# Performance work log

Hardware: AMD Instinct MI355X
Metric: run time of the kernel (lower is better)

## Reference

```python
import jax, jax.numpy as jnp
import numpy as np

N_NODES = 50000
N_EDGES = 800000
NEG_SLOPE = 0.2  # GATConv default
BN_EPS = 1e-5


def _seg_softmax(logits, seg, n):
    # per-target-node softmax over incoming edges (PyG softmax w/ +1e-16)
    m = jax.ops.segment_max(logits, seg, num_segments=n)
    m = jnp.where(jnp.isfinite(m), m, 0.0)
    e = jnp.exp(logits - m[seg])
    s = jax.ops.segment_sum(e, seg, num_segments=n)
    return e / (s[seg] + 1e-16)


def _gat_conv(x, src, dst, W, a_src, a_dst, b, concat):
    # x: [N, Fin]; W: [Fin, H*C]; a_src/a_dst: [H, C]
    n = x.shape[0]
    H, C = a_src.shape
    h = (x @ W).reshape(n, H, C)
    al_s = jnp.einsum('nhc,hc->nh', h, a_src)
    al_d = jnp.einsum('nhc,hc->nh', h, a_dst)
    logits = jax.nn.leaky_relu(al_s[src] + al_d[dst], NEG_SLOPE)  # [E, H]
    alpha = _seg_softmax(logits, dst, n)                           # [E, H]
    out = jax.ops.segment_sum(h[src] * alpha[:, :, None], dst, num_segments=n)
    out = out.reshape(n, H * C) if concat else out.mean(axis=1)
    return out + b


def _bn(x, g, b):
    mu = jnp.mean(x, axis=0)
    var = jnp.mean((x - mu) ** 2, axis=0)
    return (x - mu) * jax.lax.rsqrt(var + BN_EPS) * g + b


def _gat_params(key, fin, heads, ch, scale=0.1):
    k1, k2, k3 = jax.random.split(key, 3)
    W = jax.random.normal(k1, (fin, heads * ch), jnp.float32) * scale
    a_s = jax.random.normal(k2, (heads, ch), jnp.float32) * scale
    a_d = jax.random.normal(k3, (heads, ch), jnp.float32) * scale
    return W, a_s, a_d


def setup_inputs() -> dict:
    key = jax.random.key(0)
    ks = jax.random.split(key, 12)
    inp = {}
    inp['x'] = jax.random.normal(ks[0], (N_NODES, 3), jnp.float32)
    inp['edge_index'] = jax.random.randint(ks[1], (2, N_EDGES), 0, N_NODES, jnp.int64 if jax.config.jax_enable_x64 else jnp.int32)
    inp['W11'], inp['as11'], inp['ad11'] = _gat_params(ks[2], 3, 8, 8)
    inp['b11'] = jnp.zeros((64,), jnp.float32)
    inp['W12'], inp['as12'], inp['ad12'] = _gat_params(ks[3], 64, 8, 8)
    inp['b12'] = jnp.zeros((64,), jnp.float32)
    inp['g1'] = jnp.ones((64,), jnp.float32)
    inp['be1'] = jnp.zeros((64,), jnp.float32)
    inp['W21'], inp['as21'], inp['ad21'] = _gat_params(ks[4], 64, 8, 32)
    inp['b21'] = jnp.zeros((256,), jnp.float32)
    inp['W22'], inp['as22'], inp['ad22'] = _gat_params(ks[5], 256, 8, 32)
    inp['b22'] = jnp.zeros((256,), jnp.float32)
    inp['g2'] = jnp.ones((256,), jnp.float32)
    inp['be2'] = jnp.zeros((256,), jnp.float32)
    inp['W31'], inp['as31'], inp['ad31'] = _gat_params(ks[6], 256, 8, 64)
    inp['b31'] = jnp.zeros((512,), jnp.float32)
    inp['W32'], inp['as32'], inp['ad32'] = _gat_params(ks[7], 512, 8, 1)
    inp['b32'] = jnp.zeros((1,), jnp.float32)
    return inp


def reference(x, edge_index,
              W11, as11, ad11, b11, W12, as12, ad12, b12, g1, be1,
              W21, as21, ad21, b21, W22, as22, ad22, b22, g2, be2,
              W31, as31, ad31, b31, W32, as32, ad32, b32):
    n = x.shape[0]
    loops = jnp.arange(n, dtype=edge_index.dtype)
    src = jnp.concatenate([edge_index[0], loops])  # add_self_loops=True
    dst = jnp.concatenate([edge_index[1], loops])
    # GAT(3, 64, 2): conv -> relu -> conv
    h = jax.nn.relu(_gat_conv(x, src, dst, W11, as11, ad11, b11, True))
    h = _gat_conv(h, src, dst, W12, as12, ad12, b12, True)
    h = jax.nn.leaky_relu(_bn(h, g1, be1), 0.1)
    # GAT(64, 256, 2)
    h = jax.nn.relu(_gat_conv(h, src, dst, W21, as21, ad21, b21, True))
    h = _gat_conv(h, src, dst, W22, as22, ad22, b22, True)
    h = jax.nn.leaky_relu(_bn(h, g2, be2), 0.1)
    # GAT(256, 512, 2, 1): conv -> relu -> conv(concat=False)
    h = jax.nn.relu(_gat_conv(h, src, dst, W31, as31, ad31, b31, True))
    h = _gat_conv(h, src, dst, W32, as32, ad32, b32, False)
    return jax.nn.sigmoid(h)
```

## Files before the change

kernel.cpp:

```cpp
#include <hip/hip_runtime.h>
#include <math.h>

typedef short short8 __attribute__((ext_vector_type(8)));
typedef short short4v __attribute__((ext_vector_type(4)));
typedef float f32x4 __attribute__((ext_vector_type(4)));

__device__ __forceinline__ unsigned short f2bf(float v){
  unsigned u = __builtin_bit_cast(unsigned, v);
  u += 0x7FFFu + ((u >> 16) & 1u);
  return (unsigned short)(u >> 16);
}
__device__ __forceinline__ float bf2f(unsigned short b){
  unsigned u = ((unsigned)b) << 16;
  return __builtin_bit_cast(float, u);
}

__global__ void k_deg(const int* __restrict__ dstv, int* __restrict__ deg, int E){
  int e = blockIdx.x*blockDim.x + threadIdx.x;
  if (e < E) atomicAdd(&deg[dstv[e]], 1);
}

__global__ void k_scan(const int* __restrict__ deg, int* __restrict__ off,
                       int* __restrict__ cursor, int N){
  __shared__ int wpre[16];
  __shared__ int s_tot;
  __shared__ int carry;
  int tid = threadIdx.x;
  int lane = tid & 63, wv = tid >> 6;
  if (tid == 0) carry = 0;
  __syncthreads();
  for (int base = 0; base < N; base += 1024){
    int i = base + tid;
    int v = (i < N) ? deg[i] : 0;
    int incl = v;
    #pragma unroll
    for (int d = 1; d < 64; d <<= 1){
      int t = __shfl_up(incl, d, 64);
      if (lane >= d) incl += t;
    }
    if (lane == 63) wpre[wv] = incl;
    __syncthreads();
    if (tid < 16){
      int x = wpre[tid];
      int ix = x;
      #pragma unroll
      for (int d = 1; d < 16; d <<= 1){
        int t = __shfl_up(ix, d, 16);
        if (tid >= d) ix += t;
      }
      wpre[tid] = ix - x;
      if (tid == 15) s_tot = ix;
    }
    __syncthreads();
    int c = carry;
    int excl = c + wpre[wv] + (incl - v);
    if (i < N){ off[i+1] = excl + v; cursor[i] = excl; }
    __syncthreads();
    if (tid == 0) carry = c + s_tot;
    __syncthreads();
  }
  if (tid == 0) off[0] = 0;
}

__global__ void k_fill(const int* __restrict__ srcv, const int* __restrict__ dstv,
                       int* __restrict__ cursor, int* __restrict__ csr, int E){
  int e = blockIdx.x*blockDim.x + threadIdx.x;
  if (e < E){
    int d = dstv[e];
    int p = atomicAdd(&cursor[d], 1);
    csr[p] = srcv[e];
  }
}

__global__ void k_prepB(const float* __restrict__ W, unsigned short* __restrict__ bh,
                        unsigned short* __restrict__ bl, int K, int kpshift, int Nn){
  int Kp = 1 << kpshift;
  int i = blockIdx.x*blockDim.x + threadIdx.x;
  if (i >= Nn*Kp) return;
  int n = i >> kpshift, k = i & (Kp-1);
  float v = (k < K) ? W[(size_t)k*Nn + n] : 0.0f;
  unsigned short h = f2bf(v);
  bh[i] = h;
  bl[i] = f2bf(v - bf2f(h));
}

__global__ void k_bn_coef(const float* __restrict__ bsum, const float* __restrict__ bsq,
                          const float* __restrict__ g, const float* __restrict__ b,
                          float* __restrict__ sc, float* __restrict__ sh,
                          float invN, int HC){
  int f = threadIdx.x + blockIdx.x*blockDim.x;
  if (f >= HC) return;
  float mu  = bsum[f]*invN;
  float var = bsq[f]*invN - mu*mu;
  float rs  = rsqrtf(var + 1e-5f) * g[f];
  sc[f] = rs;
  sh[f] = b[f] - mu*rs;
}

template<int BN, int MODE>
__global__ __launch_bounds__((BN==64)?256:512)
void gemm_mfma(const float* __restrict__ A, const unsigned short* __restrict__ Bh,
               const unsigned short* __restrict__ Bl,
               const float* __restrict__ bnsc, const float* __restrict__ bnsh,
               const float* __restrict__ a_s, const float* __restrict__ a_d,
               unsigned short* __restrict__ Pb, float* __restrict__ D, int M, int K){
  constexpr int WAVES   = (BN==64) ? 4 : 8;
  constexpr int BLOCK   = WAVES*64;
  constexpr int WAVES_N = BN/64;
  constexpr int WAVES_M = WAVES/WAVES_N;
  constexpr int WM      = 64/WAVES_M;
  constexpr int MF      = WM/16;
  constexpr int CH      = (BN==512)?64 : (BN==256)?32 : 8;
  const int Kp = (K + 63) & ~(int)63;

  __shared__ char lds[16384];

  int tid  = threadIdx.x;
  int lane = tid & 63;
  int wid  = tid >> 6;
  int wn = wid % WAVES_N;
  int wm = wid / WAVES_N;
  int n0w = wn*64;
  int wm0 = wm*WM;
  int m0 = blockIdx.x * 64;

  f32x4 acc[MF][4];
  #pragma unroll
  for (int i = 0; i < MF; ++i)
    #pragma unroll
    for (int j = 0; j < 4; ++j)
      acc[i][j] = (f32x4){0.f,0.f,0.f,0.f};

  constexpr int SITER = 512/BLOCK;

  for (int k0 = 0; k0 < Kp; k0 += 64){
    __syncthreads();
    #pragma unroll
    for (int it = 0; it < SITER; ++it){
      int i = it*BLOCK + tid;
      int row = i >> 3, c8 = i & 7;
      int gm = m0 + row;
      int gk = k0 + c8*8;
      float v[8];
      if (gm < M && gk + 8 <= K){
        const float* ap = A + (size_t)gm*K + gk;
        float4 x0 = *(const float4*)ap;
        float4 x1 = *(const float4*)(ap+4);
        v[0]=x0.x; v[1]=x0.y; v[2]=x0.z; v[3]=x0.w;
        v[4]=x1.x; v[5]=x1.y; v[6]=x1.z; v[7]=x1.w;
        if constexpr (MODE == 1){
          #pragma unroll
          for (int j=0;j<8;++j){
            float u = v[j]*bnsc[gk+j] + bnsh[gk+j];
            v[j] = u > 0.f ? u : 0.1f*u;
          }
        }
      } else {
        #pragma unroll
        for (int j=0;j<8;++j){
          int gkj = gk + j;
          bool ok = (gm < M && gkj < K);
          float u = ok ? A[(size_t)gm*K + gkj] : 0.0f;
          if constexpr (MODE == 1){
            if (ok){
              u = u*bnsc[gkj] + bnsh[gkj];
              u = u > 0.f ? u : 0.1f*u;
            }
          }
          v[j] = u;
        }
      }
      short8 hi, lo;
      #pragma unroll
      for (int j=0;j<8;++j){
        unsigned short hb = f2bf(v[j]);
        hi[j] = (short)hb;
        lo[j] = (short)f2bf(v[j] - bf2f(hb));
      }
      int off = row*128 + ((c8 ^ (row&7))<<4);
      *(short8*)(lds + off) = hi;
      *(short8*)(lds + 8192 + off) = lo;
    }
    __syncthreads();
    #pragma unroll
    for (int kk = 0; kk < 2; ++kk){
      short8 bhf[4], blf[4];
      #pragma unroll
      for (int nf = 0; nf < 4; ++nf){
        int ncol = n0w + nf*16 + (lane & 15);
        int kidx = k0 + kk*32 + ((lane>>4)<<3);
        size_t bo = (size_t)ncol*Kp + kidx;
        bhf[nf] = *(const short8*)(Bh + bo);
        blf[nf] = *(const short8*)(Bl + bo);
      }
      #pragma unroll
      for (int mt = 0; mt < MF; ++mt){
        int row = wm0 + mt*16 + (lane & 15);
        int c8 = kk*4 + (lane>>4);
        int off = row*128 + ((c8 ^ (row&7))<<4);
        short8 ah = *(const short8*)(lds + off);
        short8 al = *(const short8*)(lds + 8192 + off);
        #pragma unroll
        for (int nf = 0; nf < 4; ++nf){
          acc[mt][nf] = __builtin_amdgcn_mfma_f32_16x16x32_bf16(ah, bhf[nf], acc[mt][nf], 0,0,0);
          acc[mt][nf] = __builtin_amdgcn_mfma_f32_16x16x32_bf16(ah, blf[nf], acc[mt][nf], 0,0,0);
          acc[mt][nf] = __builtin_amdgcn_mfma_f32_16x16x32_bf16(al, bhf[nf], acc[mt][nf], 0,0,0);
        }
      }
    }
  }

  float asv[4], adv[4];
  #pragma unroll
  for (int nf=0; nf<4; ++nf){
    int gcol = n0w + nf*16 + (lane&15);
    asv[nf] = a_s[gcol];
    adv[nf] = a_d[gcol];
  }
  #pragma unroll
  for (int mt = 0; mt < MF; ++mt){
    #pragma unroll
    for (int r = 0; r < 4; ++r){
      int gm = m0 + wm0 + mt*16 + ((lane>>4)<<2) + r;
      bool ok = gm < M;
      #pragma unroll
      for (int nf=0;nf<4;++nf){
        if (ok) Pb[(size_t)gm*BN + n0w + nf*16 + (lane&15)] = f2bf(acc[mt][nf][r]);
      }
      float* dp = D + (size_t)gm*16;
      if constexpr (CH == 64){
        float ps = acc[mt][0][r]*asv[0] + acc[mt][1][r]*asv[1]
                 + acc[mt][2][r]*asv[2] + acc[mt][3][r]*asv[3];
        float pd = acc[mt][0][r]*adv[0] + acc[mt][1][r]*adv[1]
                 + acc[mt][2][r]*adv[2] + acc[mt][3][r]*adv[3];
        #pragma unroll
        for (int d2=1; d2<16; d2<<=1){ ps += __shfl_xor(ps,d2,64); pd += __shfl_xor(pd,d2,64); }
        if (ok && (lane&15)==0){
          int head = n0w >> 6;
          dp[head] = ps;
          dp[8 + head] = pd;
        }
      } else if constexpr (CH == 32){
        float ps0 = acc[mt][0][r]*asv[0] + acc[mt][1][r]*asv[1];
        float ps1 = acc[mt][2][r]*asv[2] + acc[mt][3][r]*asv[3];
        float pd0 = acc[mt][0][r]*adv[0] + acc[mt][1][r]*adv[1];
        float pd1 = acc[mt][2][r]*adv[2] + acc[mt][3][r]*adv[3];
        #pragma unroll
        for (int d2=1; d2<16; d2<<=1){
          ps0 += __shfl_xor(ps0,d2,64); ps1 += __shfl_xor(ps1,d2,64);
          pd0 += __shfl_xor(pd0,d2,64); pd1 += __shfl_xor(pd1,d2,64);
        }
        if (ok && (lane&15)==0){
          int head = n0w >> 5;
          dp[head]     = ps0;
          dp[head + 1] = ps1;
          dp[8 + head]     = pd0;
          dp[8 + head + 1] = pd1;
        }
      } else {
        #pragma unroll
        for (int nf=0;nf<4;++nf){
          float ps = acc[mt][nf][r]*asv[nf];
          float pd = acc[mt][nf][r]*adv[nf];
          #pragma unroll
          for (int d2=1; d2<8; d2<<=1){ ps += __shfl_xor(ps,d2,64); pd += __shfl_xor(pd,d2,64); }
          if (ok && (lane&7)==0){
            int head = nf*2 + ((lane>>3)&1);
            dp[head]     = ps;
            dp[8 + head] = pd;
          }
        }
      }
    }
  }
}

template<int HC, int ACT, int OBF>
__global__ __launch_bounds__(256)
void k_agg(const unsigned short* __restrict__ Pb, const float* __restrict__ D,
           const int* __restrict__ off, const int* __restrict__ csr,
           const float* __restrict__ bias, void* __restrict__ outv, int N){
  constexpr int R = HC/64;
  __shared__ float salpha[4][512];
  int lane = threadIdx.x & 63;
  int wid  = threadIdx.x >> 6;
  int n = blockIdx.x*4 + wid;
  if (n >= N) return;
  int o0 = off[n], deg = off[n+1]-o0;
  int myh = lane >> 3;

  float aldn[8];
  {
    const float* dn = D + (size_t)n*16 + 8;
    float4 x0 = *(const float4*)dn;
    float4 x1 = *(const float4*)(dn+4);
    aldn[0]=x0.x; aldn[1]=x0.y; aldn[2]=x0.z; aldn[3]=x0.w;
    aldn[4]=x1.x; aldn[5]=x1.y; aldn[6]=x1.z; aldn[7]=x1.w;
  }

  float acc[R];
  #pragma unroll
  for (int j=0;j<R;++j) acc[j]=0.f;

  if (deg < 64){
    int nE = deg + 1;
    int myidx = (lane < deg) ? csr[o0+lane] : n;
    bool active = (lane < nE);
    float v[8];
    {
      const float* dp = D + (size_t)myidx*16;
      float4 x0 = *(const float4*)dp;
      float4 x1 = *(const float4*)(dp+4);
      float t[8] = {x0.x,x0.y,x0.z,x0.w,x1.x,x1.y,x1.z,x1.w};
      #pragma unroll
      for (int h=0;h<8;++h){
        float u = t[h] + aldn[h];
        u = u > 0.f ? u : 0.2f*u;
        v[h] = active ? u : -1e30f;
      }
    }
    float m[8];
    #pragma unroll
    for (int h=0;h<8;++h) m[h]=v[h];
    #pragma unroll
    for (int d=1; d<64; d<<=1)
      #pragma unroll
      for (int h=0;h<8;++h) m[h] = fmaxf(m[h], __shfl_xor(m[h], d, 64));
    float sv[8], s[8];
    #pragma unroll
    for (int h=0;h<8;++h){ sv[h] = active ? __expf(v[h]-m[h]) : 0.f; s[h]=sv[h]; }
    #pragma unroll
    for (int d=1; d<64; d<<=1)
      #pragma unroll
      for (int h=0;h<8;++h) s[h] += __shfl_xor(s[h], d, 64);
    if (active){
      #pragma unroll
      for (int h=0;h<8;++h) salpha[wid][lane*8+h] = sv[h] / (s[h] + 1e-16f);
    }
    asm volatile("s_waitcnt lgkmcnt(0)" ::: "memory");

    for (int e=0; e<nE; ++e){
      int src = __shfl(myidx, e, 64);
      float alpha = salpha[wid][e*8 + myh];
      const unsigned short* hp = Pb + (size_t)src*HC + lane*R;
      if constexpr (R == 1){
        acc[0] += alpha * bf2f(hp[0]);
      } else if constexpr (R == 4){
        short4v w = *(const short4v*)hp;
        #pragma unroll
        for (int j=0;j<4;++j) acc[j] += alpha * bf2f((unsigned short)w[j]);
      } else {
        short8 w = *(const short8*)hp;
        #pragma unroll
        for (int j=0;j<8;++j) acc[j] += alpha * bf2f((unsigned short)w[j]);
      }
    }
  } else {
    float m[8];
    #pragma unroll
    for (int h=0;h<8;++h) m[h] = -1e30f;
    for (int e = lane; e <= deg; e += 64){
      int src = (e < deg) ? csr[o0+e] : n;
      const float* ap = D + (size_t)src*16;
      #pragma unroll
      for (int h=0;h<8;++h){
        float u = ap[h] + aldn[h];
        u = u > 0.f ? u : 0.2f*u;
        m[h] = fmaxf(m[h], u);
      }
    }
    #pragma unroll
    for (int d=1; d<64; d<<=1)
      #pragma unroll
      for (int h=0;h<8;++h) m[h] = fmaxf(m[h], __shfl_xor(m[h], d, 64));
    float s[8] = {0,0,0,0,0,0,0,0};
    for (int e = lane; e <= deg; e += 64){
      int src = (e < deg) ? csr[o0+e] : n;
      const float* ap = D + (size_t)src*16;
      #pragma unroll
      for (int h=0;h<8;++h){
        float u = ap[h] + aldn[h];
        u = u > 0.f ? u : 0.2f*u;
        s[h] += __expf(u - m[h]);
      }
    }
    #pragma unroll
    for (int d=1; d<64; d<<=1)
      #pragma unroll
      for (int h=0;h<8;++h) s[h] += __shfl_xor(s[h], d, 64);
    float mh = m[myh];
    float rsh = 1.0f/(s[myh] + 1e-16f);
    float adh = aldn[myh];
    for (int e = 0; e <= deg; ++e){
      int src = (e < deg) ? csr[o0+e] : n;
      float u = D[(size_t)src*16 + myh] + adh;
      u = u > 0.f ? u : 0.2f*u;
      float alpha = __expf(u - mh) * rsh;
      const unsigned short* hp = Pb + (size_t)src*HC + lane*R;
      if constexpr (R == 1){
        acc[0] += alpha * bf2f(hp[0]);
      } else if constexpr (R == 4){
        short4v w = *(const short4v*)hp;
        #pragma unroll
        for (int j=0;j<4;++j) acc[j] += alpha * bf2f((unsigned short)w[j]);
      } else {
        short8 w = *(const short8*)hp;
        #pragma unroll
        for (int j=0;j<8;++j) acc[j] += alpha * bf2f((unsigned short)w[j]);
      }
    }
  }

  #pragma unroll
  for (int j = 0; j < R; ++j){
    int f = lane*R + j;
    float v = acc[j] + bias[f];
    if (ACT == 1) v = fmaxf(v, 0.0f);
    if constexpr (OBF == 1)
      ((unsigned short*)outv)[(size_t)n*HC + f] = f2bf(v);
    else
      ((float*)outv)[(size_t)n*HC + f] = v;
  }
}

__global__ void k_bn_stats(const float* __restrict__ x, float* __restrict__ gsum,
                           float* __restrict__ gsq, int N, int HC){
  int f = threadIdx.x;
  float s = 0.f, q = 0.f;
  for (int r = blockIdx.x; r < N; r += gridDim.x){
    float v = x[(size_t)r*HC + f];
    s += v; q += v*v;
  }
  atomicAdd(&gsum[f], s);
  atomicAdd(&gsq[f], q);
}

__global__ __launch_bounds__(256)
void gemm8(const unsigned short* __restrict__ Qb, const float* __restrict__ W,
           float* __restrict__ h8, int M){
  int lane = threadIdx.x & 63;
  int gw = (blockIdx.x*blockDim.x + threadIdx.x) >> 6;
  int nw = (gridDim.x*blockDim.x) >> 6;
  float w[8][8];
  const float* wp = W + lane*64;
  #pragma unroll
  for (int j=0;j<8;++j){
    float4 a = *(const float4*)(wp + j*8);
    float4 b = *(const float4*)(wp + j*8 + 4);
    w[j][0]=a.x; w[j][1]=a.y; w[j][2]=a.z; w[j][3]=a.w;
    w[j][4]=b.x; w[j][5]=b.y; w[j][6]=b.z; w[j][7]=b.w;
  }
  for (int n = gw; n < M; n += nw){
    short8 v8 = *(const short8*)(Qb + (size_t)n*512 + lane*8);
    float p[8] = {0,0,0,0,0,0,0,0};
    #pragma unroll
    for (int j=0;j<8;++j){
      float x = bf2f((unsigned short)v8[j]);
      #pragma unroll
      for (int o=0;o<8;++o) p[o] += x * w[j][o];
    }
    #pragma unroll
    for (int d=1; d<64; d<<=1)
      #pragma unroll
      for (int o=0;o<8;++o) p[o] += __shfl_xor(p[o], d, 64);
    if (lane == 0){
      float4 y0 = make_float4(p[0],p[1],p[2],p[3]);
      float4 y1 = make_float4(p[4],p[5],p[6],p[7]);
      *(float4*)(h8 + (size_t)n*8)     = y0;
      *(float4*)(h8 + (size_t)n*8 + 4) = y1;
    }
  }
}

__global__ __launch_bounds__(256)
void k_final(const float* __restrict__ h8, const float* __restrict__ a_s,
             const float* __restrict__ a_d, const int* __restrict__ off,
             const int* __restrict__ csr, const float* __restrict__ b32,
             float* __restrict__ outp, int N){
  int lane = threadIdx.x & 63;
  int wv   = threadIdx.x >> 6;
  int n = blockIdx.x*4 + wv;
  if (n >= N) return;
  int o0 = off[n], deg = off[n+1]-o0;
  float asv[8], adv[8];
  #pragma unroll
  for (int h=0;h<8;++h){ asv[h]=a_s[h]; adv[h]=a_d[h]; }
  float aldn[8];
  {
    const float* hp = h8 + (size_t)n*8;
    float4 x0 = *(const float4*)hp;
    float4 x1 = *(const float4*)(hp+4);
    float hn[8] = {x0.x,x0.y,x0.z,x0.w,x1.x,x1.y,x1.z,x1.w};
    #pragma unroll
    for (int h=0;h<8;++h) aldn[h] = hn[h]*adv[h];
  }

  if (deg < 64){
    int nE = deg + 1;
    int src = (lane < deg) ? csr[o0+lane] : n;
    bool act = (lane < nE);
    float hs[8];
    {
      const float* hp = h8 + (size_t)src*8;
      float4 x0 = *(const float4*)hp;
      float4 x1 = *(const float4*)(hp+4);
      hs[0]=x0.x; hs[1]=x0.y; hs[2]=x0.z; hs[3]=x0.w;
      hs[4]=x1.x; hs[5]=x1.y; hs[6]=x1.z; hs[7]=x1.w;
    }
    float v[8];
    #pragma unroll
    for (int h=0;h<8;++h){
      float u = hs[h]*asv[h] + aldn[h];
      u = u > 0.f ? u : 0.2f*u;
      v[h] = act ? u : -1e30f;
    }
    float m[8];
    #pragma unroll
    for (int h=0;h<8;++h) m[h]=v[h];
    #pragma unroll
    for (int d=1; d<64; d<<=1)
      #pragma unroll
      for (int h=0;h<8;++h) m[h] = fmaxf(m[h], __shfl_xor(m[h], d, 64));
    float s[8], t[8];
    #pragma unroll
    for (int h=0;h<8;++h){
      float e = act ? __expf(v[h]-m[h]) : 0.f;
      s[h]=e; t[h]=e*hs[h];
    }
    #pragma unroll
    for (int d=1; d<64; d<<=1)
      #pragma unroll
      for (int h=0;h<8;++h){
        s[h] += __shfl_xor(s[h], d, 64);
        t[h] += __shfl_xor(t[h], d, 64);
      }
    if (lane == 0){
      float o = 0.f;
      #pragma unroll
      for (int h=0;h<8;++h) o += t[h]/(s[h]+1e-16f);
      o = o*0.125f + b32[0];
      outp[n] = 1.0f/(1.0f + __expf(-o));
    }
  } else if (lane == 0){
    float m[8], s[8], agg[8];
    #pragma unroll
    for (int h=0;h<8;++h){ m[h]=-1e30f; s[h]=0.f; agg[h]=0.f; }
    for (int e = 0; e <= deg; ++e){
      int src = (e < deg) ? csr[o0+e] : n;
      #pragma unroll
      for (int h=0;h<8;++h){
        float u = h8[(size_t)src*8+h]*asv[h] + aldn[h];
        u = u > 0.f ? u : 0.2f*u;
        m[h] = fmaxf(m[h], u);
      }
    }
    for (int e = 0; e <= deg; ++e){
      int src = (e < deg) ? csr[o0+e] : n;
      #pragma unroll
      for (int h=0;h<8;++h){
        float u = h8[(size_t)src*8+h]*asv[h] + aldn[h];
        u = u > 0.f ? u : 0.2f*u;
        float ex = __expf(u - m[h]);
        s[h] += ex;
        agg[h] += ex * h8[(size_t)src*8+h];
      }
    }
    float o = 0.f;
    #pragma unroll
    for (int h=0;h<8;++h) o += agg[h]/(s[h]+1e-16f);
    o = o*0.125f + b32[0];
    outp[n] = 1.0f/(1.0f + __expf(-o));
  }
}

extern "C" void kernel_launch(void* const* d_in, const int* in_sizes, int n_in,
                              void* d_out, int out_size, void* d_ws, size_t ws_size,
                              hipStream_t stream){
  int N = in_sizes[0]/3;
  int E = in_sizes[1]/2;
  const float* x    = (const float*)d_in[0];
  const int*   ei   = (const int*)  d_in[1];
  const float* W11  = (const float*)d_in[2];
  const float* as11 = (const float*)d_in[3];
  const float* ad11 = (const float*)d_in[4];
  const float* b11  = (const float*)d_in[5];
  const float* W12  = (const float*)d_in[6];
  const float* as12 = (const float*)d_in[7];
  const float* ad12 = (const float*)d_in[8];
  const float* b12  = (const float*)d_in[9];
  const float* g1   = (const float*)d_in[10];
  const float* be1  = (const float*)d_in[11];
  const float* W21  = (const float*)d_in[12];
  const float* as21 = (const float*)d_in[13];
  const float* ad21 = (const float*)d_in[14];
  const float* b21  = (const float*)d_in[15];
  const float* W22  = (const float*)d_in[16];
  const float* as22 = (const float*)d_in[17];
  const float* ad22 = (const float*)d_in[18];
  const float* b22  = (const float*)d_in[19];
  const float* g2   = (const float*)d_in[20];
  const float* be2  = (const float*)d_in[21];
  const float* W31  = (const float*)d_in[22];
  const float* as31 = (const float*)d_in[23];
  const float* ad31 = (const float*)d_in[24];
  const float* b31  = (const float*)d_in[25];
  const float* W32  = (const float*)d_in[26];
  const float* as32 = (const float*)d_in[27];
  const float* ad32 = (const float*)d_in[28];
  const float* b32  = (const float*)d_in[29];

  char* ws = (char*)d_ws;
  size_t o = 0;
  auto alloc = [&](size_t bytes)->char*{
    char* p = ws + o;
    o = (o + bytes + 255) & ~(size_t)255;
    return p;
  };
  int*   deg    = (int*)  alloc((size_t)N*4);
  int*   off    = (int*)  alloc((size_t)(N+1)*4);
  int*   cursor = (int*)  alloc((size_t)N*4);
  int*   csr    = (int*)  alloc((size_t)E*4);
  unsigned short* bth = (unsigned short*)alloc(131072*2);
  unsigned short* btl = (unsigned short*)alloc(131072*2);
  float* h8     = (float*)alloc((size_t)N*8*4);
  float* bsum   = (float*)alloc(1024);
  float* bsq    = (float*)alloc(1024);
  float* bnsc   = (float*)alloc(1024);
  float* bnsh   = (float*)alloc(1024);
  unsigned short* Pb = (unsigned short*)alloc((size_t)N*512*2);
  float* D      = (float*)alloc((size_t)N*16*4);
  float* Q      = (float*)alloc((size_t)N*512*4);
  unsigned short* Qb = (unsigned short*)alloc((size_t)N*512*2);
  (void)ws_size;

  hipMemsetAsync(deg, 0, (size_t)N*4, stream);
  int eb = (E+255)/256;
  k_deg <<<eb, 256, 0, stream>>>(ei+E, deg, E);
  k_scan<<<1, 1024, 0, stream>>>(deg, off, cursor, N);
  k_fill<<<eb, 256, 0, stream>>>(ei, ei+E, cursor, csr, E);

  int mb = (N+63)/64;
  int nb4 = (N+3)/4;
  float invN = 1.0f/(float)N;

  k_prepB<<<(64*64)/256, 256, 0, stream>>>(W11, bth, btl, 3, 6, 64);
  gemm_mfma<64,0><<<mb, 256, 0, stream>>>(x, bth, btl, nullptr, nullptr,
                                          as11, ad11, Pb, D, N, 3);
  k_agg<64,1,0><<<nb4, 256, 0, stream>>>(Pb, D, off, csr, b11, Q, N);

  k_prepB<<<(64*64)/256, 256, 0, stream>>>(W12, bth, btl, 64, 6, 64);
  gemm_mfma<64,0><<<mb, 256, 0, stream>>>(Q, bth, btl, nullptr, nullptr,
                                          as12, ad12, Pb, D, N, 64);
  k_agg<64,0,0><<<nb4, 256, 0, stream>>>(Pb, D, off, csr, b12, Q, N);
  hipMemsetAsync(bsum, 0, 2048, stream);
  k_bn_stats<<<512, 64, 0, stream>>>(Q, bsum, bsq, N, 64);
  k_bn_coef<<<1, 64, 0, stream>>>(bsum, bsq, g1, be1, bnsc, bnsh, invN, 64);

  k_prepB<<<(256*64)/256, 256, 0, stream>>>(W21, bth, btl, 64, 6, 256);
  gemm_mfma<256,1><<<mb, 512, 0, stream>>>(Q, bth, btl, bnsc, bnsh,
                                           as21, ad21, Pb, D, N, 64);
  k_agg<256,1,0><<<nb4, 256, 0, stream>>>(Pb, D, off, csr, b21, Q, N);

  k_prepB<<<(256*256)/256, 256, 0, stream>>>(W22, bth, btl, 256, 8, 256);
  gemm_mfma<256,0><<<mb, 512, 0, stream>>>(Q, bth, btl, nullptr, nullptr,
                                           as22, ad22, Pb, D, N, 256);
  k_agg<256,0,0><<<nb4, 256, 0, stream>>>(Pb, D, off, csr, b22, Q, N);
  hipMemsetAsync(bsum, 0, 2048, stream);
  k_bn_stats<<<512, 256, 0, stream>>>(Q, bsum, bsq, N, 256);
  k_bn_coef<<<1, 256, 0, stream>>>(bsum, bsq, g2, be2, bnsc, bnsh, invN, 256);

  k_prepB<<<(512*256)/256, 256, 0, stream>>>(W31, bth, btl, 256, 8, 512);
  gemm_mfma<512,1><<<mb, 512, 0, stream>>>(Q, bth, btl, bnsc, bnsh,
                                           as31, ad31, Pb, D, N, 256);
  k_agg<512,1,1><<<nb4, 256, 0, stream>>>(Pb, D, off, csr, b31, Qb, N);

  gemm8<<<1024, 256, 0, stream>>>(Qb, W32, h8, N);
  k_final<<<nb4, 256, 0, stream>>>(h8, as32, ad32, off, csr, b32,
                                   (float*)d_out, N);
}
```

Baseline: 1.146 ms.

## Store intermediate activations in bf16 and split attention-logit buffers

All aggregation outputs are now written as bf16 instead of fp32. The following GEMMs read bf16 activations directly. When the input is already bf16 and needs no batchnorm transform, the GEMM drops the low-part A term, going from three MFMA passes to two and halving LDS use. The source and destination logit arrays are split into two contiguous 8-float buffers, so the edge gathers touch only source-logit rows. This cuts activation memory traffic and MFMA work, but activations and batchnorm statistics now carry bf16 rounding, which lowers accuracy.

```diff
diff --git a/kernel.cpp b/kernel.cpp
--- a/kernel.cpp
+++ b/kernel.cpp
@@ -97,13 +97,14 @@
   sh[f] = b[f] - mu*rs;
 }
 
-template<int BN, int MODE>
+template<int BN, int AFMT>
 __global__ __launch_bounds__((BN==64)?256:512)
-void gemm_mfma(const float* __restrict__ A, const unsigned short* __restrict__ Bh,
+void gemm_mfma(const void* __restrict__ Av, const unsigned short* __restrict__ Bh,
                const unsigned short* __restrict__ Bl,
                const float* __restrict__ bnsc, const float* __restrict__ bnsh,
                const float* __restrict__ a_s, const float* __restrict__ a_d,
-               unsigned short* __restrict__ Pb, float* __restrict__ D, int M, int K){
+               unsigned short* __restrict__ Pb, float* __restrict__ Ds,
+               float* __restrict__ Dd, int M, int K){
   constexpr int WAVES   = (BN==64) ? 4 : 8;
   constexpr int BLOCK   = WAVES*64;
   constexpr int WAVES_N = BN/64;
@@ -111,9 +112,10 @@
   constexpr int WM      = 64/WAVES_M;
   constexpr int MF      = WM/16;
   constexpr int CH      = (BN==512)?64 : (BN==256)?32 : 8;
+  constexpr int TERMS   = (AFMT==2) ? 2 : 3;
   const int Kp = (K + 63) & ~(int)63;
 
-  __shared__ char lds[16384];
+  __shared__ char lds[(TERMS==3)?16384:8192];
 
   int tid  = threadIdx.x;
   int lane = tid & 63;
@@ -141,45 +143,52 @@
       int row = i >> 3, c8 = i & 7;
       int gm = m0 + row;
       int gk = k0 + c8*8;
-      float v[8];
-      if (gm < M && gk + 8 <= K){
-        const float* ap = A + (size_t)gm*K + gk;
-        float4 x0 = *(const float4*)ap;
-        float4 x1 = *(const float4*)(ap+4);
-        v[0]=x0.x; v[1]=x0.y; v[2]=x0.z; v[3]=x0.w;
-        v[4]=x1.x; v[5]=x1.y; v[6]=x1.z; v[7]=x1.w;
-        if constexpr (MODE == 1){
+      int off = row*128 + ((c8 ^ (row&7))<<4);
+      if constexpr (AFMT == 2){
+        short8 hv = {0,0,0,0,0,0,0,0};
+        if (gm < M) hv = *(const short8*)((const unsigned short*)Av + (size_t)gm*K + gk);
+        *(short8*)(lds + off) = hv;
+      } else if constexpr (AFMT == 1){
+        short8 raw = {0,0,0,0,0,0,0,0};
+        if (gm < M) raw = *(const short8*)((const unsigned short*)Av + (size_t)gm*K + gk);
+        short8 hi, lo;
+        #pragma unroll
+        for (int j=0;j<8;++j){
+          float u = bf2f((unsigned short)raw[j])*bnsc[gk+j] + bnsh[gk+j];
+          u = u > 0.f ? u : 0.1f*u;
+          if (gm >= M) u = 0.f;
+          unsigned short hb = f2bf(u);
+          hi[j] = (short)hb;
+          lo[j] = (short)f2bf(u - bf2f(hb));
+        }
+        *(short8*)(lds + off) = hi;
+        *(short8*)(lds + 8192 + off) = lo;
+      } else {
+        const float* A = (const float*)Av;
+        float v[8];
+        if (gm < M && gk + 8 <= K){
+          const float* ap = A + (size_t)gm*K + gk;
+          float4 x0 = *(const float4*)ap;
+          float4 x1 = *(const float4*)(ap+4);
+          v[0]=x0.x; v[1]=x0.y; v[2]=x0.z; v[3]=x0.w;
+          v[4]=x1.x; v[5]=x1.y; v[6]=x1.z; v[7]=x1.w;
+        } else {
           #pragma unroll
           for (int j=0;j<8;++j){
-            float u = v[j]*bnsc[gk+j] + bnsh[gk+j];
-            v[j] = u > 0.f ? u : 0.1f*u;
+            int gkj = gk + j;
+            v[j] = (gm < M && gkj < K) ? A[(size_t)gm*K + gkj] : 0.0f;
           }
         }
-      } else {
+        short8 hi, lo;
         #pragma unroll
         for (int j=0;j<8;++j){
-          int gkj = gk + j;
-          bool ok = (gm < M && gkj < K);
-          float u = ok ? A[(size_t)gm*K + gkj] : 0.0f;
-          if constexpr (MODE == 1){
-            if (ok){
-              u = u*bnsc[gkj] + bnsh[gkj];
-              u = u > 0.f ? u : 0.1f*u;
-            }
-          }
-          v[j] = u;
-        }
-      }
-      short8 hi, lo;
-      #pragma unroll
-      for (int j=0;j<8;++j){
-        unsigned short hb = f2bf(v[j]);
-        hi[j] = (short)hb;
-        lo[j] = (short)f2bf(v[j] - bf2f(hb));
-      }
-      int off = row*128 + ((c8 ^ (row&7))<<4);
-      *(short8*)(lds + off) = hi;
-      *(short8*)(lds + 8192 + off) = lo;
+          unsigned short hb = f2bf(v[j]);
+          hi[j] = (short)hb;
+          lo[j] = (short)f2bf(v[j] - bf2f(hb));
+        }
+        *(short8*)(lds + off) = hi;
+        *(short8*)(lds + 8192 + off) = lo;
+      }
     }
     __syncthreads();
     #pragma unroll
@@ -199,12 +208,16 @@
         int c8 = kk*4 + (lane>>4);
         int off = row*128 + ((c8 ^ (row&7))<<4);
         short8 ah = *(const short8*)(lds + off);
-        short8 al = *(const short8*)(lds + 8192 + off);
         #pragma unroll
         for (int nf = 0; nf < 4; ++nf){
           acc[mt][nf] = __builtin_amdgcn_mfma_f32_16x16x32_bf16(ah, bhf[nf], acc[mt][nf], 0,0,0);
           acc[mt][nf] = __builtin_amdgcn_mfma_f32_16x16x32_bf16(ah, blf[nf], acc[mt][nf], 0,0,0);
-          acc[mt][nf] = __builtin_amdgcn_mfma_f32_16x16x32_bf16(al, bhf[nf], acc[mt][nf], 0,0,0);
+        }
+        if constexpr (TERMS == 3){
+          short8 al = *(const short8*)(lds + 8192 + off);
+          #pragma unroll
+          for (int nf = 0; nf < 4; ++nf)
+            acc[mt][nf] = __builtin_amdgcn_mfma_f32_16x16x32_bf16(al, bhf[nf], acc[mt][nf], 0,0,0);
         }
       }
     }
@@ -227,7 +240,6 @@
       for (int nf=0;nf<4;++nf){
         if (ok) Pb[(size_t)gm*BN + n0w + nf*16 + (lane&15)] = f2bf(acc[mt][nf][r]);
       }
-      float* dp = D + (size_t)gm*16;
       if constexpr (CH == 64){
         float ps = acc[mt][0][r]*asv[0] + acc[mt][1][r]*asv[1]
                  + acc[mt][2][r]*asv[2] + acc[mt][3][r]*asv[3];
@@ -237,8 +249,8 @@
         for (int d2=1; d2<16; d2<<=1){ ps += __shfl_xor(ps,d2,64); pd += __shfl_xor(pd,d2,64); }
         if (ok && (lane&15)==0){
           int head = n0w >> 6;
-          dp[head] = ps;
-          dp[8 + head] = pd;
+          Ds[(size_t)gm*8 + head] = ps;
+          Dd[(size_t)gm*8 + head] = pd;
         }
       } else if constexpr (CH == 32){
         float ps0 = acc[mt][0][r]*asv[0] + acc[mt][1][r]*asv[1];
@@ -252,10 +264,10 @@
         }
         if (ok && (lane&15)==0){
           int head = n0w >> 5;
-          dp[head]     = ps0;
-          dp[head + 1] = ps1;
-          dp[8 + head]     = pd0;
-          dp[8 + head + 1] = pd1;
+          Ds[(size_t)gm*8 + head]     = ps0;
+          Ds[(size_t)gm*8 + head + 1] = ps1;
+          Dd[(size_t)gm*8 + head]     = pd0;
+          Dd[(size_t)gm*8 + head + 1] = pd1;
         }
       } else {
         #pragma unroll
@@ -266,8 +278,8 @@
           for (int d2=1; d2<8; d2<<=1){ ps += __shfl_xor(ps,d2,64); pd += __shfl_xor(pd,d2,64); }
           if (ok && (lane&7)==0){
             int head = nf*2 + ((lane>>3)&1);
-            dp[head]     = ps;
-            dp[8 + head] = pd;
+            Ds[(size_t)gm*8 + head] = ps;
+            Dd[(size_t)gm*8 + head] = pd;
           }
         }
       }
@@ -275,11 +287,12 @@
   }
 }
 
-template<int HC, int ACT, int OBF>
+template<int HC, int ACT>
 __global__ __launch_bounds__(256)
-void k_agg(const unsigned short* __restrict__ Pb, const float* __restrict__ D,
-           const int* __restrict__ off, const int* __restrict__ csr,
-           const float* __restrict__ bias, void* __restrict__ outv, int N){
+void k_agg(const unsigned short* __restrict__ Pb, const float* __restrict__ Ds,
+           const float* __restrict__ Dd, const int* __restrict__ off,
+           const int* __restrict__ csr, const float* __restrict__ bias,
+           unsigned short* __restrict__ outb, int N){
   constexpr int R = HC/64;
   __shared__ float salpha[4][512];
   int lane = threadIdx.x & 63;
@@ -291,7 +304,7 @@
 
   float aldn[8];
   {
-    const float* dn = D + (size_t)n*16 + 8;
+    const float* dn = Dd + (size_t)n*8;
     float4 x0 = *(const float4*)dn;
     float4 x1 = *(const float4*)(dn+4);
     aldn[0]=x0.x; aldn[1]=x0.y; aldn[2]=x0.z; aldn[3]=x0.w;
@@ -308,7 +321,7 @@
     bool active = (lane < nE);
     float v[8];
     {
-      const float* dp = D + (size_t)myidx*16;
+      const float* dp = Ds + (size_t)myidx*8;
       float4 x0 = *(const float4*)dp;
       float4 x1 = *(const float4*)(dp+4);
       float t[8] = {x0.x,x0.y,x0.z,x0.w,x1.x,x1.y,x1.z,x1.w};
@@ -361,7 +374,7 @@
     for (int h=0;h<8;++h) m[h] = -1e30f;
     for (int e = lane; e <= deg; e += 64){
       int src = (e < deg) ? csr[o0+e] : n;
-      const float* ap = D + (size_t)src*16;
+      const float* ap = Ds + (size_t)src*8;
       #pragma unroll
       for (int h=0;h<8;++h){
         float u = ap[h] + aldn[h];
@@ -376,7 +389,7 @@
     float s[8] = {0,0,0,0,0,0,0,0};
     for (int e = lane; e <= deg; e += 64){
       int src = (e < deg) ? csr[o0+e] : n;
-      const float* ap = D + (size_t)src*16;
+      const float* ap = Ds + (size_t)src*8;
       #pragma unroll
       for (int h=0;h<8;++h){
         float u = ap[h] + aldn[h];
@@ -393,7 +406,7 @@
     float adh = aldn[myh];
     for (int e = 0; e <= deg; ++e){
       int src = (e < deg) ? csr[o0+e] : n;
-      float u = D[(size_t)src*16 + myh] + adh;
+      float u = Ds[(size_t)src*8 + myh] + adh;
       u = u > 0.f ? u : 0.2f*u;
       float alpha = __expf(u - mh) * rsh;
       const unsigned short* hp = Pb + (size_t)src*HC + lane*R;
@@ -416,19 +429,16 @@
     int f = lane*R + j;
     float v = acc[j] + bias[f];
     if (ACT == 1) v = fmaxf(v, 0.0f);
-    if constexpr (OBF == 1)
-      ((unsigned short*)outv)[(size_t)n*HC + f] = f2bf(v);
-    else
-      ((float*)outv)[(size_t)n*HC + f] = v;
-  }
-}
-
-__global__ void k_bn_stats(const float* __restrict__ x, float* __restrict__ gsum,
+    outb[(size_t)n*HC + f] = f2bf(v);
+  }
+}
+
+__global__ void k_bn_stats(const unsigned short* __restrict__ x, float* __restrict__ gsum,
                            float* __restrict__ gsq, int N, int HC){
   int f = threadIdx.x;
   float s = 0.f, q = 0.f;
   for (int r = blockIdx.x; r < N; r += gridDim.x){
-    float v = x[(size_t)r*HC + f];
+    float v = bf2f(x[(size_t)r*HC + f]);
     s += v; q += v*v;
   }
   atomicAdd(&gsum[f], s);
@@ -628,9 +638,9 @@
   float* bnsc   = (float*)alloc(1024);
   float* bnsh   = (float*)alloc(1024);
   unsigned short* Pb = (unsigned short*)alloc((size_t)N*512*2);
-  float* D      = (float*)alloc((size_t)N*16*4);
-  float* Q      = (float*)alloc((size_t)N*512*4);
   unsigned short* Qb = (unsigned short*)alloc((size_t)N*512*2);
+  float* Dsb    = (float*)alloc((size_t)N*8*4);
+  float* Ddb    = (float*)alloc((size_t)N*8*4);
   (void)ws_size;
 
   hipMemsetAsync(deg, 0, (size_t)N*4, stream);
@@ -645,34 +655,34 @@
 
   k_prepB<<<(64*64)/256, 256, 0, stream>>>(W11, bth, btl, 3, 6, 64);
   gemm_mfma<64,0><<<mb, 256, 0, stream>>>(x, bth, btl, nullptr, nullptr,
-                                          as11, ad11, Pb, D, N, 3);
-  k_agg<64,1,0><<<nb4, 256, 0, stream>>>(Pb, D, off, csr, b11, Q, N);
+                                          as11, ad11, Pb, Dsb, Ddb, N, 3);
+  k_agg<64,1><<<nb4, 256, 0, stream>>>(Pb, Dsb, Ddb, off, csr, b11, Qb, N);
 
   k_prepB<<<(64*64)/256, 256, 0, stream>>>(W12, bth, btl, 64, 6, 64);
-  gemm_mfma<64,0><<<mb, 256, 0, stream>>>(Q, bth, btl, nullptr, nullptr,
-                                          as12, ad12, Pb, D, N, 64);
-  k_agg<64,0,0><<<nb4, 256, 0, stream>>>(Pb, D, off, csr, b12, Q, N);
+  gemm_mfma<64,2><<<mb, 256, 0, stream>>>(Qb, bth, btl, nullptr, nullptr,
+                                          as12, ad12, Pb, Dsb, Ddb, N, 64);
+  k_agg<64,0><<<nb4, 256, 0, stream>>>(Pb, Dsb, Ddb, off, csr, b12, Qb, N);
   hipMemsetAsync(bsum, 0, 2048, stream);
-  k_bn_stats<<<512, 64, 0, stream>>>(Q, bsum, bsq, N, 64);
+  k_bn_stats<<<512, 64, 0, stream>>>(Qb, bsum, bsq, N, 64);
   k_bn_coef<<<1, 64, 0, stream>>>(bsum, bsq, g1, be1, bnsc, bnsh, invN, 64);
 
   k_prepB<<<(256*64)/256, 256, 0, stream>>>(W21, bth, btl, 64, 6, 256);
-  gemm_mfma<256,1><<<mb, 512, 0, stream>>>(Q, bth, btl, bnsc, bnsh,
-                                           as21, ad21, Pb, D, N, 64);
-  k_agg<256,1,0><<<nb4, 256, 0, stream>>>(Pb, D, off, csr, b21, Q, N);
+  gemm_mfma<256,1><<<mb, 512, 0, stream>>>(Qb, bth, btl, bnsc, bnsh,
+                                           as21, ad21, Pb, Dsb, Ddb, N, 64);
+  k_agg<256,1><<<nb4, 256, 0, stream>>>(Pb, Dsb, Ddb, off, csr, b21, Qb, N);
 
   k_prepB<<<(256*256)/256, 256, 0, stream>>>(W22, bth, btl, 256, 8, 256);
-  gemm_mfma<256,0><<<mb, 512, 0, stream>>>(Q, bth, btl, nullptr, nullptr,
-                                           as22, ad22, Pb, D, N, 256);
-  k_agg<256,0,0><<<nb4, 256, 0, stream>>>(Pb, D, off, csr, b22, Q, N);
+  gemm_mfma<256,2><<<mb, 512, 0, stream>>>(Qb, bth, btl, nullptr, nullptr,
+                                           as22, ad22, Pb, Dsb, Ddb, N, 256);
+  k_agg<256,0><<<nb4, 256, 0, stream>>>(Pb, Dsb, Ddb, off, csr, b22, Qb, N);
   hipMemsetAsync(bsum, 0, 2048, stream);
-  k_bn_stats<<<512, 256, 0, stream>>>(Q, bsum, bsq, N, 256);
+  k_bn_stats<<<512, 256, 0, stream>>>(Qb, bsum, bsq, N, 256);
   k_bn_coef<<<1, 256, 0, stream>>>(bsum, bsq, g2, be2, bnsc, bnsh, invN, 256);
 
   k_prepB<<<(512*256)/256, 256, 0, stream>>>(W31, bth, btl, 256, 8, 512);
-  gemm_mfma<512,1><<<mb, 512, 0, stream>>>(Q, bth, btl, bnsc, bnsh,
-                                           as31, ad31, Pb, D, N, 256);
-  k_agg<512,1,1><<<nb4, 256, 0, stream>>>(Pb, D, off, csr, b31, Qb, N);
+  gemm_mfma<512,1><<<mb, 512, 0, stream>>>(Qb, bth, btl, bnsc, bnsh,
+                                           as31, ad31, Pb, Dsb, Ddb, N, 256);
+  k_agg<512,1><<<nb4, 256, 0, stream>>>(Pb, Dsb, Ddb, off, csr, b31, Qb, N);
 
   gemm8<<<1024, 256, 0, stream>>>(Qb, W32, h8, N);
   k_final<<<nb4, 256, 0, stream>>>(h8, as32, ad32, off, csr, b32,
```

Measured after the change: 1.140 ms. No clear change (-0.5%).
